# Performance work log

Hardware: AMD Instinct MI355X
Metric: run time of the kernel (lower is better)

Reference implementation:

```python
import jax, jax.numpy as jnp
import numpy as np

N, M_CTX, SIN, YDIM, SPROJ = 16384, 4096, 256, 7, 256


def setup_inputs() -> dict:
    key = jax.random.key(0)
    k1, k2, k3, k4, k5 = jax.random.split(key, 5)
    return {
        "x": jax.random.normal(k1, (N, SIN), dtype=jnp.float32),
        "y": jax.random.normal(k2, (M_CTX, YDIM), dtype=jnp.float32),
        "Wq": jax.random.normal(k3, (SIN, SPROJ), dtype=jnp.float32) / np.sqrt(SIN),
        "Wk": jax.random.normal(k4, (YDIM, SPROJ), dtype=jnp.float32) / np.sqrt(YDIM),
        "Wv": jax.random.normal(k5, (YDIM, SPROJ), dtype=jnp.float32) / np.sqrt(YDIM),
    }


def smooth_softmax(x):
    # softmax over keys (axis=1) blended with 0.1*relu, renormalized
    s = jax.nn.softmax(x, axis=1)
    num = jax.nn.relu(x) * 0.1 + s
    return num / jnp.sum(num, axis=1, keepdims=True)


def reference(x, y, Wq, Wk, Wv):
    XQ = x @ Wq            # [N, P]
    YK = y @ Wk            # [M, P]
    YV = y @ Wv            # [M, P]
    scores = (XQ @ YK.T) / jnp.sqrt(jnp.asarray(YK.shape[1], XQ.dtype))  # [N, M]
    A = smooth_softmax(scores)
    return A @ YV          # [N, P]
```

## Files before the change

kernel.cpp:

```cpp
#include <hip/hip_runtime.h>
#include <hip/hip_bf16.h>

#define N_Q   16384
#define MCTX  4096
#define DSIN  256
#define YDIM  7
#define PDIM  256
#define BK    32

typedef __attribute__((ext_vector_type(8))) short s16x8;
typedef __attribute__((ext_vector_type(4))) float f32x4;
typedef unsigned short u16;

static __device__ __forceinline__ u16 f2bf(float f) {
    union { float f; unsigned u; } v; v.f = f;
    unsigned r = v.u + 0x7fffu + ((v.u >> 16) & 1u);
    return (u16)(r >> 16);
}
static __device__ __forceinline__ float bf2f(u16 h) {
    union { unsigned u; float f; } v; v.u = ((unsigned)h) << 16;
    return v.f;
}
static __device__ __forceinline__ f32x4 mfma16(s16x8 a, s16x8 b, f32x4 c) {
    return __builtin_amdgcn_mfma_f32_16x16x32_bf16(a, b, c, 0, 0, 0);
}
static __device__ __forceinline__ void gload_lds16(const u16* g, u16* l) {
    __builtin_amdgcn_global_load_lds(
        (const __attribute__((address_space(1))) unsigned int*)(g),
        (__attribute__((address_space(3))) unsigned int*)(l), 16, 0, 0);
}
static __device__ __forceinline__ void block_barrier() {
    asm volatile("" ::: "memory");
    __builtin_amdgcn_s_barrier();
    asm volatile("" ::: "memory");
    __builtin_amdgcn_sched_barrier(0);
}

__global__ void k_prep(const float* __restrict__ Wq, u16* __restrict__ WtH,
                       u16* __restrict__ WtL, const float* __restrict__ y,
                       const float* __restrict__ Wk, const float* __restrict__ Wv,
                       u16* __restrict__ YK, u16* __restrict__ YVb) {
    if (blockIdx.x < PDIM) {
        int n = blockIdx.x;
        int k = threadIdx.x;
        float w = Wq[(size_t)k * PDIM + n];
        u16 h = f2bf(w);
        WtH[(size_t)n * DSIN + k] = h;
        WtL[(size_t)n * DSIN + k] = f2bf(w - bf2f(h));
    } else {
        int kb = blockIdx.x - PDIM;
        int p  = threadIdx.x;
        float wk[YDIM], wv[YDIM];
#pragma unroll
        for (int j = 0; j < YDIM; ++j) {
            wk[j] = Wk[(size_t)j * PDIM + p];
            wv[j] = Wv[(size_t)j * PDIM + p];
        }
        u16 vbuf[32];
#pragma unroll
        for (int m = 0; m < 32; ++m) {
            int key = kb * 32 + m;
            float ak = 0.f, av = 0.f;
#pragma unroll
            for (int j = 0; j < YDIM; ++j) {
                float yy = y[(size_t)key * YDIM + j];
                ak += yy * wk[j];
                av += yy * wv[j];
            }
            YK[(size_t)key * PDIM + p] = f2bf(ak * 0.0625f);
            vbuf[m] = f2bf(av);
        }
        s16x8* dst = (s16x8*)(YVb + ((size_t)kb * PDIM + p) * 32);
#pragma unroll
        for (int c = 0; c < 4; ++c) dst[c] = ((s16x8*)vbuf)[c];
    }
}

__global__ __launch_bounds__(256, 2) void k_xq(const float* __restrict__ x,
                                               const u16* __restrict__ WtH,
                                               const u16* __restrict__ WtL,
                                               u16* __restrict__ XQ) {
    __shared__ u16 xH[32 * 256];
    __shared__ u16 xL[32 * 256];
    const int tid = threadIdx.x;
    const int rowg0 = blockIdx.x * 32;

#pragma unroll
    for (int i = 0; i < 4; ++i) {
        int row = (tid >> 5) + i * 8;
        int c32 = tid & 31;
        const float* px = x + (size_t)(rowg0 + row) * DSIN + c32 * 8;
        float4 a = *(const float4*)px;
        float4 b = *(const float4*)(px + 4);
        float vals[8] = {a.x, a.y, a.z, a.w, b.x, b.y, b.z, b.w};
        s16x8 h, l;
#pragma unroll
        for (int j = 0; j < 8; ++j) {
            u16 hh = f2bf(vals[j]);
            h[j] = (short)hh;
            l[j] = (short)f2bf(vals[j] - bf2f(hh));
        }
        int pc = c32 ^ (row & 7);
        *(s16x8*)(xH + row * 256 + pc * 8) = h;
        *(s16x8*)(xL + row * 256 + pc * 8) = l;
    }
    __syncthreads();

    const int wave = tid >> 6, lane = tid & 63;
    const int quad = lane >> 4, m16 = lane & 15;
    const int rh = wave & 1, ph = wave >> 1;
    const int rowl = rh * 16 + m16;
    const int swz = rowl & 7;
    s16x8 ah[8], al[8];
#pragma unroll
    for (int kf = 0; kf < 8; ++kf) {
        int pc = (kf * 4 + quad) ^ swz;
        ah[kf] = *(const s16x8*)(xH + rowl * 256 + pc * 8);
        al[kf] = *(const s16x8*)(xL + rowl * 256 + pc * 8);
    }
#pragma unroll
    for (int ptl = 0; ptl < 8; ++ptl) {
        int pt = ph * 8 + ptl;
        f32x4 acc = (f32x4){0.f, 0.f, 0.f, 0.f};
#pragma unroll
        for (int kf = 0; kf < 8; ++kf) {
            size_t idx = (size_t)(pt * 16 + m16) * DSIN + kf * 32 + quad * 8;
            s16x8 bh = *(const s16x8*)(WtH + idx);
            s16x8 bl = *(const s16x8*)(WtL + idx);
            acc = mfma16(ah[kf], bh, acc);
            acc = mfma16(al[kf], bh, acc);
            acc = mfma16(ah[kf], bl, acc);
        }
#pragma unroll
        for (int r = 0; r < 4; ++r)
            XQ[(size_t)(rowg0 + rh * 16 + quad * 4 + r) * PDIM + pt * 16 + m16] =
                f2bf(acc[r]);
    }
}

__global__ __launch_bounds__(256, 2) void k_attn(const u16* __restrict__ XQ,
                                                 const u16* __restrict__ YK,
                                                 const u16* __restrict__ YVb,
                                                 u16* __restrict__ accE,
                                                 u16* __restrict__ accR,
                                                 float* __restrict__ lsum,
                                                 float* __restrict__ rsum,
                                                 int msPerSplit) {
    __shared__ u16 Kt[2][32 * 256];
    __shared__ u16 Pe[64 * 40];
    __shared__ u16 Pr[64 * 40];

    const int tid = threadIdx.x;
    const int wave = tid >> 6, lane = tid & 63;
    const int quad = lane >> 4, m16 = lane & 15;
    const int split = blockIdx.y;
    const int qbase = blockIdx.x * 64;
    const int key_begin = split * msPerSplit;
    const int iters = msPerSplit / BK;
    const int pslice = wave * 64;
    const int swz = m16 & 7;

    s16x8 qf[8];
    const u16* qp = XQ + (size_t)(qbase + wave * 16 + m16) * DSIN;
#pragma unroll
    for (int kf = 0; kf < 8; ++kf)
        qf[kf] = *(const s16x8*)(qp + kf * 32 + quad * 8);

    f32x4 aE[4][4], aR[4][4];
#pragma unroll
    for (int g = 0; g < 4; ++g)
#pragma unroll
        for (int t = 0; t < 4; ++t) {
            aE[g][t] = (f32x4){0.f, 0.f, 0.f, 0.f};
            aR[g][t] = (f32x4){0.f, 0.f, 0.f, 0.f};
        }
    float lacc[4] = {0.f, 0.f, 0.f, 0.f}, racc[4] = {0.f, 0.f, 0.f, 0.f};

    auto stage = [&](int key0, int buf) {
#pragma unroll
        for (int c = 0; c < 4; ++c) {
            int l = (wave * 4 + c) * 64 + lane;
            int r = l >> 5;
            int sc = (l & 31) ^ (r & 7);
            gload_lds16(YK + (size_t)(key0 + r) * DSIN + sc * 8,
                        &Kt[buf][(size_t)(wave * 4 + c) * 512]);
        }
    };
    stage(key_begin, 0);

    for (int it = 0; it < iters; ++it) {
        const int key0 = key_begin + it * BK;
        const int cur = it & 1;

        if (it + 1 < iters) {
            stage(key0 + BK, cur ^ 1);
            asm volatile("s_waitcnt vmcnt(4)" ::: "memory");
        } else {
            asm volatile("s_waitcnt vmcnt(0)" ::: "memory");
        }
        __builtin_amdgcn_sched_barrier(0);
        block_barrier();

        f32x4 s0 = (f32x4){0.f, 0.f, 0.f, 0.f};
        f32x4 s1 = (f32x4){0.f, 0.f, 0.f, 0.f};
        __builtin_amdgcn_s_setprio(1);
#pragma unroll
        for (int kf = 0; kf < 8; ++kf) {
            int pc = (kf * 4 + quad) ^ swz;
            s16x8 b0 = *(const s16x8*)(&Kt[cur][m16 * 256 + pc * 8]);
            s16x8 b1 = *(const s16x8*)(&Kt[cur][(16 + m16) * 256 + pc * 8]);
            s0 = mfma16(qf[kf], b0, s0);
            s1 = mfma16(qf[kf], b1, s1);
        }
        __builtin_amdgcn_s_setprio(0);
#pragma unroll
        for (int r = 0; r < 4; ++r) {
            float e0 = __expf(s0[r]), e1 = __expf(s1[r]);
            float rl0 = fmaxf(s0[r], 0.f), rl1 = fmaxf(s1[r], 0.f);
            lacc[r] += e0 + e1;
            racc[r] += rl0 + rl1;
            int row = wave * 16 + quad * 4 + r;
            Pe[row * 40 + m16]      = f2bf(e0);
            Pe[row * 40 + 16 + m16] = f2bf(e1);
            Pr[row * 40 + m16]      = f2bf(rl0);
            Pr[row * 40 + 16 + m16] = f2bf(rl1);
        }
        asm volatile("s_waitcnt lgkmcnt(0)" ::: "memory");
        __builtin_amdgcn_sched_barrier(0);
        block_barrier();

        s16x8 vf[4];
        const u16* vb = YVb + (size_t)((key0 >> 5) * PDIM) * 32;
#pragma unroll
        for (int t = 0; t < 4; ++t)
            vf[t] = *(const s16x8*)(vb + (size_t)(pslice + t * 16 + m16) * 32 + quad * 8);

        __builtin_amdgcn_s_setprio(1);
#pragma unroll
        for (int g = 0; g < 4; ++g) {
            s16x8 pa = *(const s16x8*)(Pe + (g * 16 + m16) * 40 + quad * 8);
            s16x8 pb = *(const s16x8*)(Pr + (g * 16 + m16) * 40 + quad * 8);
#pragma unroll
            for (int t = 0; t < 4; ++t) {
                aE[g][t] = mfma16(pa, vf[t], aE[g][t]);
                aR[g][t] = mfma16(pb, vf[t], aR[g][t]);
            }
        }
        __builtin_amdgcn_s_setprio(0);
    }

    size_t ob = ((size_t)split * N_Q + qbase) * PDIM;
#pragma unroll
    for (int g = 0; g < 4; ++g)
#pragma unroll
        for (int t = 0; t < 4; ++t)
#pragma unroll
            for (int r = 0; r < 4; ++r) {
                size_t o = ob + (size_t)(g * 16 + quad * 4 + r) * PDIM + pslice + t * 16 + m16;
                accE[o] = f2bf(aE[g][t][r]);
                accR[o] = f2bf(aR[g][t][r]);
            }
#pragma unroll
    for (int r = 0; r < 4; ++r) {
        lacc[r] += __shfl_xor(lacc[r], 1);
        lacc[r] += __shfl_xor(lacc[r], 2);
        lacc[r] += __shfl_xor(lacc[r], 4);
        lacc[r] += __shfl_xor(lacc[r], 8);
        racc[r] += __shfl_xor(racc[r], 1);
        racc[r] += __shfl_xor(racc[r], 2);
        racc[r] += __shfl_xor(racc[r], 4);
        racc[r] += __shfl_xor(racc[r], 8);
    }
    if (m16 < 4) {
        float lv = (m16 == 0) ? lacc[0] : (m16 == 1) ? lacc[1] : (m16 == 2) ? lacc[2] : lacc[3];
        float rv = (m16 == 0) ? racc[0] : (m16 == 1) ? racc[1] : (m16 == 2) ? racc[2] : racc[3];
        int row = split * N_Q + qbase + wave * 16 + quad * 4 + m16;
        lsum[row] = lv;
        rsum[row] = rv;
    }
}

__global__ void k_comb(const u16* __restrict__ accE, const u16* __restrict__ accR,
                       const float* __restrict__ lsum, const float* __restrict__ rsum,
                       float* __restrict__ out, int nsplit) {
    int row = blockIdx.x * 8 + (threadIdx.x >> 5);
    int col = (threadIdx.x & 31) * 8;
    size_t idx = (size_t)row * PDIM + col;
    const size_t NP = (size_t)N_Q * PDIM;
    float E[8] = {0.f, 0.f, 0.f, 0.f, 0.f, 0.f, 0.f, 0.f};
    float R[8] = {0.f, 0.f, 0.f, 0.f, 0.f, 0.f, 0.f, 0.f};
    float L = 0.f, Rs = 0.f;
    for (int s = 0; s < nsplit; ++s) {
        s16x8 e = *(const s16x8*)(accE + s * NP + idx);
        s16x8 r = *(const s16x8*)(accR + s * NP + idx);
#pragma unroll
        for (int j = 0; j < 8; ++j) {
            E[j] += bf2f((u16)e[j]);
            R[j] += bf2f((u16)r[j]);
        }
        L  += lsum[(size_t)s * N_Q + row];
        Rs += rsum[(size_t)s * N_Q + row];
    }
    float invL = 1.f / L, invD = 1.f / (1.f + 0.1f * Rs);
    float4 o0, o1;
    o0.x = (0.1f * R[0] + E[0] * invL) * invD;
    o0.y = (0.1f * R[1] + E[1] * invL) * invD;
    o0.z = (0.1f * R[2] + E[2] * invL) * invD;
    o0.w = (0.1f * R[3] + E[3] * invL) * invD;
    o1.x = (0.1f * R[4] + E[4] * invL) * invD;
    o1.y = (0.1f * R[5] + E[5] * invL) * invD;
    o1.z = (0.1f * R[6] + E[6] * invL) * invD;
    o1.w = (0.1f * R[7] + E[7] * invL) * invD;
    *(float4*)(out + idx) = o0;
    *(float4*)(out + idx + 4) = o1;
}

extern "C" void kernel_launch(void* const* d_in, const int* in_sizes, int n_in,
                              void* d_out, int out_size, void* d_ws, size_t ws_size,
                              hipStream_t stream) {
    const float* x  = (const float*)d_in[0];
    const float* y  = (const float*)d_in[1];
    const float* Wq = (const float*)d_in[2];
    const float* Wk = (const float*)d_in[3];
    const float* Wv = (const float*)d_in[4];
    float* out = (float*)d_out;

    char* ws = (char*)d_ws;
    size_t off = 0;
    auto take = [&](size_t bytes) -> char* {
        char* p = ws + off;
        off += (bytes + 255) & ~(size_t)255;
        return p;
    };
    u16* XQ  = (u16*)take((size_t)N_Q * PDIM * 2);
    u16* WtH = (u16*)take((size_t)PDIM * DSIN * 2);
    u16* WtL = (u16*)take((size_t)PDIM * DSIN * 2);
    u16* YK  = (u16*)take((size_t)MCTX * PDIM * 2);
    u16* YVb = (u16*)take((size_t)MCTX * PDIM * 2);

    size_t perSplit = (size_t)N_Q * PDIM * 2 * 2 + (size_t)N_Q * 4 * 2 + 1024;
    int nsplit = (ws_size >= off + 2 * perSplit + 4096) ? 2 : 1;

    u16*   accE = (u16*)take((size_t)nsplit * N_Q * PDIM * 2);
    u16*   accR = (u16*)take((size_t)nsplit * N_Q * PDIM * 2);
    float* lsum = (float*)take((size_t)nsplit * N_Q * 4);
    float* rsum = (float*)take((size_t)nsplit * N_Q * 4);

    hipLaunchKernelGGL(k_prep, dim3(PDIM + MCTX/32), dim3(256), 0, stream,
                       Wq, WtH, WtL, y, Wk, Wv, YK, YVb);
    hipLaunchKernelGGL(k_xq,   dim3(N_Q/32),   dim3(256),  0, stream, x, WtH, WtL, XQ);
    hipLaunchKernelGGL(k_attn, dim3(N_Q/64, nsplit), dim3(256), 0, stream,
                       XQ, YK, YVb, accE, accR, lsum, rsum, MCTX / nsplit);
    hipLaunchKernelGGL(k_comb, dim3(N_Q/8),    dim3(256),  0, stream,
                       accE, accR, lsum, rsum, out, nsplit);
}
```

Baseline: 241.6 us.

## Split attention into row-sum pass and single fused P·V pass

Adds a separate pre-pass kernel that computes the exp and relu row sums over all keys. The main kernel then folds the softmax normalisation into a single combined weight matrix, so one P·V MFMA accumulation replaces the two separate E and R accumulations. V is now stored transposed and staged into LDS alongside K through async global-to-LDS loads, and the P fragments are exchanged with register shuffles instead of going through LDS. The cost is computing QK^T twice, since the pre-pass repeats the score GEMM, and the explicit vmcnt pipelining and setprio hints are dropped in favour of a plain __syncthreads.

```diff
diff --git a/kernel.cpp b/kernel.cpp
--- a/kernel.cpp
+++ b/kernel.cpp
@@ -21,6 +21,9 @@
     union { unsigned u; float f; } v; v.u = ((unsigned)h) << 16;
     return v.f;
 }
+static __device__ __forceinline__ unsigned pack2bf(float lo, float hi) {
+    return ((unsigned)f2bf(hi) << 16) | (unsigned)f2bf(lo);
+}
 static __device__ __forceinline__ f32x4 mfma16(s16x8 a, s16x8 b, f32x4 c) {
     return __builtin_amdgcn_mfma_f32_16x16x32_bf16(a, b, c, 0, 0, 0);
 }
@@ -29,17 +32,11 @@
         (const __attribute__((address_space(1))) unsigned int*)(g),
         (__attribute__((address_space(3))) unsigned int*)(l), 16, 0, 0);
 }
-static __device__ __forceinline__ void block_barrier() {
-    asm volatile("" ::: "memory");
-    __builtin_amdgcn_s_barrier();
-    asm volatile("" ::: "memory");
-    __builtin_amdgcn_sched_barrier(0);
-}
 
 __global__ void k_prep(const float* __restrict__ Wq, u16* __restrict__ WtH,
                        u16* __restrict__ WtL, const float* __restrict__ y,
                        const float* __restrict__ Wk, const float* __restrict__ Wv,
-                       u16* __restrict__ YK, u16* __restrict__ YVb) {
+                       u16* __restrict__ YK, u16* __restrict__ YVt) {
     if (blockIdx.x < PDIM) {
         int n = blockIdx.x;
         int k = threadIdx.x;
@@ -70,7 +67,7 @@
             YK[(size_t)key * PDIM + p] = f2bf(ak * 0.0625f);
             vbuf[m] = f2bf(av);
         }
-        s16x8* dst = (s16x8*)(YVb + ((size_t)kb * PDIM + p) * 32);
+        s16x8* dst = (s16x8*)(YVt + (size_t)p * MCTX + kb * 32);
 #pragma unroll
         for (int c = 0; c < 4; ++c) dst[c] = ((s16x8*)vbuf)[c];
     }
@@ -84,7 +81,6 @@
     __shared__ u16 xL[32 * 256];
     const int tid = threadIdx.x;
     const int rowg0 = blockIdx.x * 32;
-
 #pragma unroll
     for (int i = 0; i < 4; ++i) {
         int row = (tid >> 5) + i * 8;
@@ -138,17 +134,12 @@
     }
 }
 
-__global__ __launch_bounds__(256, 2) void k_attn(const u16* __restrict__ XQ,
-                                                 const u16* __restrict__ YK,
-                                                 const u16* __restrict__ YVb,
-                                                 u16* __restrict__ accE,
-                                                 u16* __restrict__ accR,
-                                                 float* __restrict__ lsum,
-                                                 float* __restrict__ rsum,
-                                                 int msPerSplit) {
+__global__ __launch_bounds__(256, 4) void k_lr(const u16* __restrict__ XQ,
+                                               const u16* __restrict__ YK,
+                                               float* __restrict__ Lp,
+                                               float* __restrict__ Rp,
+                                               int msPerSplit) {
     __shared__ u16 Kt[2][32 * 256];
-    __shared__ u16 Pe[64 * 40];
-    __shared__ u16 Pr[64 * 40];
 
     const int tid = threadIdx.x;
     const int wave = tid >> 6, lane = tid & 63;
@@ -157,7 +148,6 @@
     const int qbase = blockIdx.x * 64;
     const int key_begin = split * msPerSplit;
     const int iters = msPerSplit / BK;
-    const int pslice = wave * 64;
     const int swz = m16 & 7;
 
     s16x8 qf[8];
@@ -165,16 +155,6 @@
 #pragma unroll
     for (int kf = 0; kf < 8; ++kf)
         qf[kf] = *(const s16x8*)(qp + kf * 32 + quad * 8);
-
-    f32x4 aE[4][4], aR[4][4];
-#pragma unroll
-    for (int g = 0; g < 4; ++g)
-#pragma unroll
-        for (int t = 0; t < 4; ++t) {
-            aE[g][t] = (f32x4){0.f, 0.f, 0.f, 0.f};
-            aR[g][t] = (f32x4){0.f, 0.f, 0.f, 0.f};
-        }
-    float lacc[4] = {0.f, 0.f, 0.f, 0.f}, racc[4] = {0.f, 0.f, 0.f, 0.f};
 
     auto stage = [&](int key0, int buf) {
 #pragma unroll
@@ -188,129 +168,165 @@
     };
     stage(key_begin, 0);
 
+    float lacc = 0.f, racc = 0.f;
     for (int it = 0; it < iters; ++it) {
-        const int key0 = key_begin + it * BK;
         const int cur = it & 1;
-
-        if (it + 1 < iters) {
-            stage(key0 + BK, cur ^ 1);
-            asm volatile("s_waitcnt vmcnt(4)" ::: "memory");
-        } else {
-            asm volatile("s_waitcnt vmcnt(0)" ::: "memory");
-        }
-        __builtin_amdgcn_sched_barrier(0);
-        block_barrier();
+        __syncthreads();
+        if (it + 1 < iters) stage(key_begin + (it + 1) * BK, cur ^ 1);
 
         f32x4 s0 = (f32x4){0.f, 0.f, 0.f, 0.f};
         f32x4 s1 = (f32x4){0.f, 0.f, 0.f, 0.f};
-        __builtin_amdgcn_s_setprio(1);
 #pragma unroll
         for (int kf = 0; kf < 8; ++kf) {
             int pc = (kf * 4 + quad) ^ swz;
             s16x8 b0 = *(const s16x8*)(&Kt[cur][m16 * 256 + pc * 8]);
             s16x8 b1 = *(const s16x8*)(&Kt[cur][(16 + m16) * 256 + pc * 8]);
-            s0 = mfma16(qf[kf], b0, s0);
-            s1 = mfma16(qf[kf], b1, s1);
-        }
-        __builtin_amdgcn_s_setprio(0);
+            s0 = mfma16(b0, qf[kf], s0);
+            s1 = mfma16(b1, qf[kf], s1);
+        }
 #pragma unroll
         for (int r = 0; r < 4; ++r) {
-            float e0 = __expf(s0[r]), e1 = __expf(s1[r]);
-            float rl0 = fmaxf(s0[r], 0.f), rl1 = fmaxf(s1[r], 0.f);
-            lacc[r] += e0 + e1;
-            racc[r] += rl0 + rl1;
-            int row = wave * 16 + quad * 4 + r;
-            Pe[row * 40 + m16]      = f2bf(e0);
-            Pe[row * 40 + 16 + m16] = f2bf(e1);
-            Pr[row * 40 + m16]      = f2bf(rl0);
-            Pr[row * 40 + 16 + m16] = f2bf(rl1);
-        }
-        asm volatile("s_waitcnt lgkmcnt(0)" ::: "memory");
-        __builtin_amdgcn_sched_barrier(0);
-        block_barrier();
-
-        s16x8 vf[4];
-        const u16* vb = YVb + (size_t)((key0 >> 5) * PDIM) * 32;
-#pragma unroll
-        for (int t = 0; t < 4; ++t)
-            vf[t] = *(const s16x8*)(vb + (size_t)(pslice + t * 16 + m16) * 32 + quad * 8);
-
-        __builtin_amdgcn_s_setprio(1);
-#pragma unroll
-        for (int g = 0; g < 4; ++g) {
-            s16x8 pa = *(const s16x8*)(Pe + (g * 16 + m16) * 40 + quad * 8);
-            s16x8 pb = *(const s16x8*)(Pr + (g * 16 + m16) * 40 + quad * 8);
-#pragma unroll
-            for (int t = 0; t < 4; ++t) {
-                aE[g][t] = mfma16(pa, vf[t], aE[g][t]);
-                aR[g][t] = mfma16(pb, vf[t], aR[g][t]);
-            }
-        }
-        __builtin_amdgcn_s_setprio(0);
+            lacc += __expf(s0[r]) + __expf(s1[r]);
+            racc += fmaxf(s0[r], 0.f) + fmaxf(s1[r], 0.f);
+        }
+    }
+    lacc += __shfl_xor(lacc, 16); lacc += __shfl_xor(lacc, 32);
+    racc += __shfl_xor(racc, 16); racc += __shfl_xor(racc, 32);
+    if (quad == 0) {
+        int row = split * N_Q + qbase + wave * 16 + m16;
+        Lp[row] = lacc;
+        Rp[row] = racc;
+    }
+}
+
+__global__ __launch_bounds__(256, 2) void k_pv(const u16* __restrict__ XQ,
+                                               const u16* __restrict__ YK,
+                                               const u16* __restrict__ YVt,
+                                               const float* __restrict__ Lp,
+                                               u16* __restrict__ Ob,
+                                               int msPerSplit) {
+    __shared__ u16 Kt[2][32 * 256];
+    __shared__ u16 Vt[2][256 * 32];
+
+    const int tid = threadIdx.x;
+    const int wave = tid >> 6, lane = tid & 63;
+    const int quad = lane >> 4, m16 = lane & 15;
+    const int split = blockIdx.y;
+    const int qbase = blockIdx.x * 64;
+    const int key_begin = split * msPerSplit;
+    const int iters = msPerSplit / BK;
+    const int swz = m16 & 7;
+
+    float Ltot = 0.f;
+#pragma unroll
+    for (int s = 0; s < 4; ++s)
+        Ltot += Lp[(size_t)s * N_Q + qbase + wave * 16 + m16];
+    const float invL = 1.f / Ltot;
+
+    s16x8 qf[8];
+    const u16* qp = XQ + (size_t)(qbase + wave * 16 + m16) * DSIN;
+#pragma unroll
+    for (int kf = 0; kf < 8; ++kf)
+        qf[kf] = *(const s16x8*)(qp + kf * 32 + quad * 8);
+
+    f32x4 acc[16];
+#pragma unroll
+    for (int pt = 0; pt < 16; ++pt) acc[pt] = (f32x4){0.f, 0.f, 0.f, 0.f};
+
+    auto stage = [&](int key0, int buf) {
+#pragma unroll
+        for (int c = 0; c < 4; ++c) {
+            int l = (wave * 4 + c) * 64 + lane;
+            int r = l >> 5;
+            int sc = (l & 31) ^ (r & 7);
+            gload_lds16(YK + (size_t)(key0 + r) * DSIN + sc * 8,
+                        &Kt[buf][(size_t)(wave * 4 + c) * 512]);
+        }
+#pragma unroll
+        for (int c = 0; c < 4; ++c) {
+            int l = (wave * 4 + c) * 64 + lane;
+            gload_lds16(YVt + (size_t)(l >> 2) * MCTX + key0 + (l & 3) * 8,
+                        &Vt[buf][(size_t)(wave * 4 + c) * 512]);
+        }
+    };
+    stage(key_begin, 0);
+
+    const int srcA = ((quad & 1) << 5) + m16;
+    const int srcB = srcA + 16;
+
+    for (int it = 0; it < iters; ++it) {
+        const int cur = it & 1;
+        __syncthreads();
+        if (it + 1 < iters) stage(key_begin + (it + 1) * BK, cur ^ 1);
+
+        f32x4 s0 = (f32x4){0.f, 0.f, 0.f, 0.f};
+        f32x4 s1 = (f32x4){0.f, 0.f, 0.f, 0.f};
+#pragma unroll
+        for (int kf = 0; kf < 8; ++kf) {
+            int pc = (kf * 4 + quad) ^ swz;
+            s16x8 b0 = *(const s16x8*)(&Kt[cur][m16 * 256 + pc * 8]);
+            s16x8 b1 = *(const s16x8*)(&Kt[cur][(16 + m16) * 256 + pc * 8]);
+            s0 = mfma16(b0, qf[kf], s0);
+            s1 = mfma16(b1, qf[kf], s1);
+        }
+        float pp[8];
+#pragma unroll
+        for (int r = 0; r < 4; ++r) {
+            pp[r]     = 0.1f * fmaxf(s0[r], 0.f) + __expf(s0[r]) * invL;
+            pp[4 + r] = 0.1f * fmaxf(s1[r], 0.f) + __expf(s1[r]) * invL;
+        }
+        unsigned w0 = pack2bf(pp[0], pp[1]);
+        unsigned w1 = pack2bf(pp[2], pp[3]);
+        unsigned w2 = pack2bf(pp[4], pp[5]);
+        unsigned w3 = pack2bf(pp[6], pp[7]);
+        int a0 = __shfl((int)w0, srcA), a1 = __shfl((int)w1, srcA);
+        int a2 = __shfl((int)w2, srcA), a3 = __shfl((int)w3, srcA);
+        int b0_ = __shfl((int)w0, srcB), b1_ = __shfl((int)w1, srcB);
+        int b2_ = __shfl((int)w2, srcB), b3_ = __shfl((int)w3, srcB);
+        const bool loq = (quad < 2);
+        union { unsigned u[4]; s16x8 v; } pa;
+        pa.u[0] = (unsigned)(loq ? a0 : a2);
+        pa.u[1] = (unsigned)(loq ? a1 : a3);
+        pa.u[2] = (unsigned)(loq ? b0_ : b2_);
+        pa.u[3] = (unsigned)(loq ? b1_ : b3_);
+
+#pragma unroll
+        for (int pt = 0; pt < 16; ++pt) {
+            s16x8 vf = *(const s16x8*)(&Vt[cur][(pt * 16 + m16) * 32 + quad * 8]);
+            acc[pt] = mfma16(pa.v, vf, acc[pt]);
+        }
     }
 
     size_t ob = ((size_t)split * N_Q + qbase) * PDIM;
 #pragma unroll
-    for (int g = 0; g < 4; ++g)
-#pragma unroll
-        for (int t = 0; t < 4; ++t)
-#pragma unroll
-            for (int r = 0; r < 4; ++r) {
-                size_t o = ob + (size_t)(g * 16 + quad * 4 + r) * PDIM + pslice + t * 16 + m16;
-                accE[o] = f2bf(aE[g][t][r]);
-                accR[o] = f2bf(aR[g][t][r]);
-            }
-#pragma unroll
-    for (int r = 0; r < 4; ++r) {
-        lacc[r] += __shfl_xor(lacc[r], 1);
-        lacc[r] += __shfl_xor(lacc[r], 2);
-        lacc[r] += __shfl_xor(lacc[r], 4);
-        lacc[r] += __shfl_xor(lacc[r], 8);
-        racc[r] += __shfl_xor(racc[r], 1);
-        racc[r] += __shfl_xor(racc[r], 2);
-        racc[r] += __shfl_xor(racc[r], 4);
-        racc[r] += __shfl_xor(racc[r], 8);
-    }
-    if (m16 < 4) {
-        float lv = (m16 == 0) ? lacc[0] : (m16 == 1) ? lacc[1] : (m16 == 2) ? lacc[2] : lacc[3];
-        float rv = (m16 == 0) ? racc[0] : (m16 == 1) ? racc[1] : (m16 == 2) ? racc[2] : racc[3];
-        int row = split * N_Q + qbase + wave * 16 + quad * 4 + m16;
-        lsum[row] = lv;
-        rsum[row] = rv;
-    }
-}
-
-__global__ void k_comb(const u16* __restrict__ accE, const u16* __restrict__ accR,
-                       const float* __restrict__ lsum, const float* __restrict__ rsum,
-                       float* __restrict__ out, int nsplit) {
+    for (int pt = 0; pt < 16; ++pt)
+#pragma unroll
+        for (int r = 0; r < 4; ++r)
+            Ob[ob + (size_t)(wave * 16 + quad * 4 + r) * PDIM + pt * 16 + m16] =
+                f2bf(acc[pt][r]);
+}
+
+__global__ void k_comb(const u16* __restrict__ Ob, const float* __restrict__ Rp,
+                       float* __restrict__ out) {
     int row = blockIdx.x * 8 + (threadIdx.x >> 5);
     int col = (threadIdx.x & 31) * 8;
     size_t idx = (size_t)row * PDIM + col;
     const size_t NP = (size_t)N_Q * PDIM;
-    float E[8] = {0.f, 0.f, 0.f, 0.f, 0.f, 0.f, 0.f, 0.f};
-    float R[8] = {0.f, 0.f, 0.f, 0.f, 0.f, 0.f, 0.f, 0.f};
-    float L = 0.f, Rs = 0.f;
-    for (int s = 0; s < nsplit; ++s) {
-        s16x8 e = *(const s16x8*)(accE + s * NP + idx);
-        s16x8 r = *(const s16x8*)(accR + s * NP + idx);
-#pragma unroll
-        for (int j = 0; j < 8; ++j) {
-            E[j] += bf2f((u16)e[j]);
-            R[j] += bf2f((u16)r[j]);
-        }
-        L  += lsum[(size_t)s * N_Q + row];
-        Rs += rsum[(size_t)s * N_Q + row];
-    }
-    float invL = 1.f / L, invD = 1.f / (1.f + 0.1f * Rs);
+    float Rs = 0.f;
+#pragma unroll
+    for (int s = 0; s < 4; ++s) Rs += Rp[(size_t)s * N_Q + row];
+    float invD = 1.f / (1.f + 0.1f * Rs);
+    s16x8 e0 = *(const s16x8*)(Ob + idx);
+    s16x8 e1 = *(const s16x8*)(Ob + NP + idx);
     float4 o0, o1;
-    o0.x = (0.1f * R[0] + E[0] * invL) * invD;
-    o0.y = (0.1f * R[1] + E[1] * invL) * invD;
-    o0.z = (0.1f * R[2] + E[2] * invL) * invD;
-    o0.w = (0.1f * R[3] + E[3] * invL) * invD;
-    o1.x = (0.1f * R[4] + E[4] * invL) * invD;
-    o1.y = (0.1f * R[5] + E[5] * invL) * invD;
-    o1.z = (0.1f * R[6] + E[6] * invL) * invD;
-    o1.w = (0.1f * R[7] + E[7] * invL) * invD;
+    o0.x = (bf2f((u16)e0[0]) + bf2f((u16)e1[0])) * invD;
+    o0.y = (bf2f((u16)e0[1]) + bf2f((u16)e1[1])) * invD;
+    o0.z = (bf2f((u16)e0[2]) + bf2f((u16)e1[2])) * invD;
+    o0.w = (bf2f((u16)e0[3]) + bf2f((u16)e1[3])) * invD;
+    o1.x = (bf2f((u16)e0[4]) + bf2f((u16)e1[4])) * invD;
+    o1.y = (bf2f((u16)e0[5]) + bf2f((u16)e1[5])) * invD;
+    o1.z = (bf2f((u16)e0[6]) + bf2f((u16)e1[6])) * invD;
+    o1.w = (bf2f((u16)e0[7]) + bf2f((u16)e1[7])) * invD;
     *(float4*)(out + idx) = o0;
     *(float4*)(out + idx + 4) = o1;
 }
@@ -332,25 +348,21 @@
         off += (bytes + 255) & ~(size_t)255;
         return p;
     };
-    u16* XQ  = (u16*)take((size_t)N_Q * PDIM * 2);
-    u16* WtH = (u16*)take((size_t)PDIM * DSIN * 2);
-    u16* WtL = (u16*)take((size_t)PDIM * DSIN * 2);
-    u16* YK  = (u16*)take((size_t)MCTX * PDIM * 2);
-    u16* YVb = (u16*)take((size_t)MCTX * PDIM * 2);
-
-    size_t perSplit = (size_t)N_Q * PDIM * 2 * 2 + (size_t)N_Q * 4 * 2 + 1024;
-    int nsplit = (ws_size >= off + 2 * perSplit + 4096) ? 2 : 1;
-
-    u16*   accE = (u16*)take((size_t)nsplit * N_Q * PDIM * 2);
-    u16*   accR = (u16*)take((size_t)nsplit * N_Q * PDIM * 2);
-    float* lsum = (float*)take((size_t)nsplit * N_Q * 4);
-    float* rsum = (float*)take((size_t)nsplit * N_Q * 4);
+    u16*   XQ  = (u16*)take((size_t)N_Q * PDIM * 2);
+    u16*   WtH = (u16*)take((size_t)PDIM * DSIN * 2);
+    u16*   WtL = (u16*)take((size_t)PDIM * DSIN * 2);
+    u16*   YK  = (u16*)take((size_t)MCTX * PDIM * 2);
+    u16*   YVt = (u16*)take((size_t)PDIM * MCTX * 2);
+    u16*   Ob  = (u16*)take((size_t)2 * N_Q * PDIM * 2);
+    float* Lpart = (float*)take((size_t)4 * N_Q * 4);
+    float* Rpart = (float*)take((size_t)4 * N_Q * 4);
 
     hipLaunchKernelGGL(k_prep, dim3(PDIM + MCTX/32), dim3(256), 0, stream,
-                       Wq, WtH, WtL, y, Wk, Wv, YK, YVb);
-    hipLaunchKernelGGL(k_xq,   dim3(N_Q/32),   dim3(256),  0, stream, x, WtH, WtL, XQ);
-    hipLaunchKernelGGL(k_attn, dim3(N_Q/64, nsplit), dim3(256), 0, stream,
-                       XQ, YK, YVb, accE, accR, lsum, rsum, MCTX / nsplit);
-    hipLaunchKernelGGL(k_comb, dim3(N_Q/8),    dim3(256),  0, stream,
-                       accE, accR, lsum, rsum, out, nsplit);
-}
+                       Wq, WtH, WtL, y, Wk, Wv, YK, YVt);
+    hipLaunchKernelGGL(k_xq,   dim3(N_Q/32), dim3(256), 0, stream, x, WtH, WtL, XQ);
+    hipLaunchKernelGGL(k_lr,   dim3(N_Q/64, 4), dim3(256), 0, stream,
+                       XQ, YK, Lpart, Rpart, MCTX / 4);
+    hipLaunchKernelGGL(k_pv,   dim3(N_Q/64, 2), dim3(256), 0, stream,
+                       XQ, YK, YVt, Lpart, Ob, MCTX / 2);
+    hipLaunchKernelGGL(k_comb, dim3(N_Q/8), dim3(256), 0, stream, Ob, Rpart, out);
+}
```

After: 270.1 us. 1.12x slower.

## Software-pipeline PV MFMAs behind next QK tile with double-buffered P

Applied to the files above, without the earlier changes.

Restructures the attention loop so the P·V MFMAs for the previous key tile run right after the QK MFMAs of the current tile. The Pe/Pr LDS buffers are double-buffered, which cuts the loop to one barrier per iteration instead of two. A final epilogue handles the last tile's P·V. This is meant to remove a barrier and overlap softmax writes with matrix work, at the cost of more LDS and simpler, less explicit vmcnt control, since the code now relies on __syncthreads.

```diff
diff --git a/kernel.cpp b/kernel.cpp
--- a/kernel.cpp
+++ b/kernel.cpp
@@ -28,12 +28,6 @@
     __builtin_amdgcn_global_load_lds(
         (const __attribute__((address_space(1))) unsigned int*)(g),
         (__attribute__((address_space(3))) unsigned int*)(l), 16, 0, 0);
-}
-static __device__ __forceinline__ void block_barrier() {
-    asm volatile("" ::: "memory");
-    __builtin_amdgcn_s_barrier();
-    asm volatile("" ::: "memory");
-    __builtin_amdgcn_sched_barrier(0);
 }
 
 __global__ void k_prep(const float* __restrict__ Wq, u16* __restrict__ WtH,
@@ -84,7 +78,6 @@
     __shared__ u16 xL[32 * 256];
     const int tid = threadIdx.x;
     const int rowg0 = blockIdx.x * 32;
-
 #pragma unroll
     for (int i = 0; i < 4; ++i) {
         int row = (tid >> 5) + i * 8;
@@ -147,8 +140,8 @@
                                                  float* __restrict__ rsum,
                                                  int msPerSplit) {
     __shared__ u16 Kt[2][32 * 256];
-    __shared__ u16 Pe[64 * 40];
-    __shared__ u16 Pr[64 * 40];
+    __shared__ u16 Pe[2][64 * 40];
+    __shared__ u16 Pr[2][64 * 40];
 
     const int tid = threadIdx.x;
     const int wave = tid >> 6, lane = tid & 63;
@@ -186,20 +179,34 @@
                         &Kt[buf][(size_t)(wave * 4 + c) * 512]);
         }
     };
+    auto pv = [&](int b, const s16x8* vf) {
+#pragma unroll
+        for (int g = 0; g < 4; ++g) {
+            s16x8 pa = *(const s16x8*)(&Pe[b][(g * 16 + m16) * 40 + quad * 8]);
+            s16x8 pb = *(const s16x8*)(&Pr[b][(g * 16 + m16) * 40 + quad * 8]);
+#pragma unroll
+            for (int t = 0; t < 4; ++t) {
+                aE[g][t] = mfma16(pa, vf[t], aE[g][t]);
+                aR[g][t] = mfma16(pb, vf[t], aR[g][t]);
+            }
+        }
+    };
+
     stage(key_begin, 0);
 
     for (int it = 0; it < iters; ++it) {
         const int key0 = key_begin + it * BK;
         const int cur = it & 1;
-
-        if (it + 1 < iters) {
-            stage(key0 + BK, cur ^ 1);
-            asm volatile("s_waitcnt vmcnt(4)" ::: "memory");
-        } else {
-            asm volatile("s_waitcnt vmcnt(0)" ::: "memory");
-        }
-        __builtin_amdgcn_sched_barrier(0);
-        block_barrier();
+        __syncthreads();
+
+        s16x8 vf[4];
+        if (it > 0) {
+            const u16* vb = YVb + (size_t)(((key0 - BK) >> 5) * PDIM) * 32;
+#pragma unroll
+            for (int t = 0; t < 4; ++t)
+                vf[t] = *(const s16x8*)(vb + (size_t)(pslice + t * 16 + m16) * 32 + quad * 8);
+        }
+        if (it + 1 < iters) stage(key0 + BK, cur ^ 1);
 
         f32x4 s0 = (f32x4){0.f, 0.f, 0.f, 0.f};
         f32x4 s1 = (f32x4){0.f, 0.f, 0.f, 0.f};
@@ -212,7 +219,9 @@
             s0 = mfma16(qf[kf], b0, s0);
             s1 = mfma16(qf[kf], b1, s1);
         }
+        if (it > 0) pv(cur ^ 1, vf);
         __builtin_amdgcn_s_setprio(0);
+
 #pragma unroll
         for (int r = 0; r < 4; ++r) {
             float e0 = __expf(s0[r]), e1 = __expf(s1[r]);
@@ -220,33 +229,23 @@
             lacc[r] += e0 + e1;
             racc[r] += rl0 + rl1;
             int row = wave * 16 + quad * 4 + r;
-            Pe[row * 40 + m16]      = f2bf(e0);
-            Pe[row * 40 + 16 + m16] = f2bf(e1);
-            Pr[row * 40 + m16]      = f2bf(rl0);
-            Pr[row * 40 + 16 + m16] = f2bf(rl1);
-        }
-        asm volatile("s_waitcnt lgkmcnt(0)" ::: "memory");
-        __builtin_amdgcn_sched_barrier(0);
-        block_barrier();
-
+            Pe[cur][row * 40 + m16]      = f2bf(e0);
+            Pe[cur][row * 40 + 16 + m16] = f2bf(e1);
+            Pr[cur][row * 40 + m16]      = f2bf(rl0);
+            Pr[cur][row * 40 + 16 + m16] = f2bf(rl1);
+        }
+    }
+
+    __syncthreads();
+    {
+        const int keyL = key_begin + (iters - 1) * BK;
+        const int bL = (iters - 1) & 1;
         s16x8 vf[4];
-        const u16* vb = YVb + (size_t)((key0 >> 5) * PDIM) * 32;
+        const u16* vb = YVb + (size_t)((keyL >> 5) * PDIM) * 32;
 #pragma unroll
         for (int t = 0; t < 4; ++t)
             vf[t] = *(const s16x8*)(vb + (size_t)(pslice + t * 16 + m16) * 32 + quad * 8);
-
-        __builtin_amdgcn_s_setprio(1);
-#pragma unroll
-        for (int g = 0; g < 4; ++g) {
-            s16x8 pa = *(const s16x8*)(Pe + (g * 16 + m16) * 40 + quad * 8);
-            s16x8 pb = *(const s16x8*)(Pr + (g * 16 + m16) * 40 + quad * 8);
-#pragma unroll
-            for (int t = 0; t < 4; ++t) {
-                aE[g][t] = mfma16(pa, vf[t], aE[g][t]);
-                aR[g][t] = mfma16(pb, vf[t], aR[g][t]);
-            }
-        }
-        __builtin_amdgcn_s_setprio(0);
+        pv(bL, vf);
     }
 
     size_t ob = ((size_t)split * N_Q + qbase) * PDIM;
@@ -348,9 +347,9 @@
 
     hipLaunchKernelGGL(k_prep, dim3(PDIM + MCTX/32), dim3(256), 0, stream,
                        Wq, WtH, WtL, y, Wk, Wv, YK, YVb);
-    hipLaunchKernelGGL(k_xq,   dim3(N_Q/32),   dim3(256),  0, stream, x, WtH, WtL, XQ);
+    hipLaunchKernelGGL(k_xq,   dim3(N_Q/32), dim3(256), 0, stream, x, WtH, WtL, XQ);
     hipLaunchKernelGGL(k_attn, dim3(N_Q/64, nsplit), dim3(256), 0, stream,
                        XQ, YK, YVb, accE, accR, lsum, rsum, MCTX / nsplit);
-    hipLaunchKernelGGL(k_comb, dim3(N_Q/8),    dim3(256),  0, stream,
+    hipLaunchKernelGGL(k_comb, dim3(N_Q/8), dim3(256), 0, stream,
                        accE, accR, lsum, rsum, out, nsplit);
 }
```

Measured after the change: 240.8 us. No clear change (-0.3%).
